# Performance work log

Hardware: AMD Instinct MI355X
Metric: run time of the kernel (lower is better)

## Reference

```python
import jax, jax.numpy as jnp
import numpy as np

IN_SHAPE = 640
LEVELS = [3, 4, 5]          # pyramid_levels [3,5] expanded
REG_LEN = 64
NUM_CLASSES = 80
MAX_OUT = 100
SCORE_TH = 0.3
IOU_TH = 0.5
NEG_INF = -1e30


def _make_anchors():
    """Anchor-free anchors: one box per grid cell, grid_zero_start=True,
    anchor_scale=1, aspect_ratio=1 -> half-size = stride/2. Normalized by input size."""
    all_a = []
    for lvl in LEVELS:
        stride = 2 ** lvl
        fs = IN_SHAPE // stride
        hh = np.arange(fs, dtype='float32') * stride
        ww = np.arange(fs, dtype='float32') * stride
        wg, hg = np.meshgrid(ww, hh)
        centers = np.stack([hg, wg], -1).reshape(-1, 2)  # [fs*fs, 2] (h, w)
        half = stride * 0.5
        all_a.append(np.concatenate([centers - half, centers + half], -1))
    return np.concatenate(all_a, 0) / IN_SHAPE  # [8400, 4]


def setup_inputs() -> dict:
    key = jax.random.key(0)
    preds = jax.random.normal(key, (64, 8400, REG_LEN + NUM_CLASSES), dtype=jnp.float32)
    anchors = jnp.asarray(_make_anchors(), dtype=jnp.float32)
    return {"preds": preds, "anchors": anchors}


def _decode_yolov8(preds, anchors):
    bbox_logits, cls_logits = preds[..., :REG_LEN], preds[..., REG_LEN:]
    B, N = bbox_logits.shape[:2]
    bins = REG_LEN // 4  # 16
    d = bbox_logits.reshape(B, N, 4, bins)
    # softmax-weighted DFL expectation over bins
    d = jnp.sum(jax.nn.softmax(d, axis=-1) * jnp.arange(bins, dtype=d.dtype), axis=-1)  # [B,N,4]
    tl, br = d[..., :2], d[..., 2:]
    anchors_hw = anchors[:, 2:] - anchors[:, :2]          # [N,2]
    anchors_ctr = (anchors[:, :2] + anchors[:, 2:]) * 0.5  # [N,2]
    bc = (br - tl) * 0.5 * anchors_hw + anchors_ctr        # center
    bhw = (br + tl) * anchors_hw                           # height/width
    boxes = jnp.concatenate([bc - bhw * 0.5, bc + bhw * 0.5], -1)  # [B,N,4] corners
    return boxes, cls_logits


def _iou_one_vs_all(box, boxes):
    tl = jnp.maximum(box[:2], boxes[:, :2])
    br = jnp.minimum(box[2:], boxes[:, 2:])
    inter = jnp.prod(jnp.clip(br - tl, 0.0, None), -1)
    a1 = jnp.prod(box[2:] - box[:2])
    a2 = jnp.prod(boxes[:, 2:] - boxes[:, :2], -1)
    return inter / (a1 + a2 - inter + 1e-9)


def _nms_single(boxes, scores):
    """Greedy hard NMS for one image. boxes [N,4], scores [N] -> idxs [MAX_OUT] (-1 = invalid)."""
    n = scores.shape[0]
    sc0 = jnp.where(scores > SCORE_TH, scores, NEG_INF)

    def step(sc, _):
        j = jnp.argmax(sc)
        valid = sc[j] > NEG_INF * 0.5
        idx = jnp.where(valid, j, -1).astype(jnp.int32)
        iou = _iou_one_vs_all(boxes[j], boxes)
        sc = jnp.where((iou > IOU_TH) | (jnp.arange(n) == j), NEG_INF, sc)
        return sc, idx

    _, idxs = jax.lax.scan(step, sc0, None, length=MAX_OUT)
    return idxs


def reference(preds, anchors):
    boxes, cls = _decode_yolov8(preds, anchors)       # [B,N,4], [B,N,C]
    scores = jnp.max(cls, -1)                          # [B,N]
    labels = jnp.argmax(cls, -1).astype(jnp.int32)     # [B,N]
    idxs = jax.vmap(_nms_single)(boxes, scores)        # [B,MAX_OUT]
    valid = idxs >= 0
    safe = jnp.maximum(idxs, 0)
    out_boxes = jnp.take_along_axis(boxes, safe[:, :, None], axis=1) * valid[..., None]
    out_scores = jnp.take_along_axis(scores, safe, axis=1) * valid
    out_labels = jnp.where(valid, jnp.take_along_axis(labels, safe, axis=1), -1)
    return out_boxes, out_labels, out_scores
```

## Files before the change

kernel.cpp:

```cpp
#include <hip/hip_runtime.h>

namespace {
constexpr int kB = 64;
constexpr int kN = 8400;
constexpr int kNP = 16384;
constexpr int kReg = 64;
constexpr int kCls = 80;
constexpr int kStride = kReg + kCls;
constexpr int kMaxOut = 100;
constexpr float kScoreTh = 0.3f;
constexpr float kIouTh = 0.5f;
}

__global__ __launch_bounds__(256) void decode2_k(
    const float* __restrict__ preds,
    const float* __restrict__ anchors,
    float4* __restrict__ boxes,
    float* __restrict__ scores,
    int* __restrict__ labels,
    unsigned long long* __restrict__ keys)
{
    __shared__ float lds[64 * 148];
    const int tid = threadIdx.x;
    const size_t gbase = (size_t)blockIdx.x * 64;

    const float4* src = (const float4*)(preds + gbase * kStride);
    float4* l4 = (float4*)lds;
#pragma unroll
    for (int k = 0; k < 9; ++k) {
        int i = tid + k * 256;
        int row = i / 36, col = i - row * 36;
        l4[row * 37 + col] = src[i];
    }
    __syncthreads();

    const int a = tid >> 2, s = tid & 3;
    const float* rowp = lds + a * 148;

    float x[16];
    const float4* q = (const float4*)(rowp + s * 16);
#pragma unroll
    for (int j = 0; j < 4; ++j) ((float4*)x)[j] = q[j];
    float m = x[0];
#pragma unroll
    for (int j = 1; j < 16; ++j) m = fmaxf(m, x[j]);
    float se = 0.f, we = 0.f;
#pragma unroll
    for (int j = 0; j < 16; ++j) {
        float t = expf(x[j] - m);
        se += t;
        we += t * (float)j;
    }
    float d = we / se;

    const float4* cl = (const float4*)(rowp + kReg + s * 20);
    float bv = -3e38f; int bi = 0;
#pragma unroll
    for (int c = 0; c < 5; ++c) {
        float4 v = cl[c];
        int cb = s * 20 + 4 * c;
        if (v.x > bv) { bv = v.x; bi = cb; }
        if (v.y > bv) { bv = v.y; bi = cb + 1; }
        if (v.z > bv) { bv = v.z; bi = cb + 2; }
        if (v.w > bv) { bv = v.w; bi = cb + 3; }
    }

    const int lane = tid & 63;
    const int base = lane & ~3;
    float d0 = __shfl(d, base + 0, 64);
    float d1 = __shfl(d, base + 1, 64);
    float d2 = __shfl(d, base + 2, 64);
    float d3 = __shfl(d, base + 3, 64);
    float v1 = __shfl(bv, base + 1, 64); int i1 = __shfl(bi, base + 1, 64);
    float v2 = __shfl(bv, base + 2, 64); int i2 = __shfl(bi, base + 2, 64);
    float v3 = __shfl(bv, base + 3, 64); int i3 = __shfl(bi, base + 3, 64);

    if (s == 0) {
        float best = bv; int bl = bi;
        if (v1 > best) { best = v1; bl = i1; }
        if (v2 > best) { best = v2; bl = i2; }
        if (v3 > best) { best = v3; bl = i3; }

        size_t gi = gbase + a;
        int bimg = (int)(gi / kN);
        int n = (int)(gi - (size_t)bimg * kN);
        float4 av = ((const float4*)anchors)[n];
        float ah0 = av.z - av.x, ah1 = av.w - av.y;
        float c0 = (av.x + av.z) * 0.5f, c1 = (av.y + av.w) * 0.5f;
        float bc0 = (d2 - d0) * 0.5f * ah0 + c0;
        float bc1 = (d3 - d1) * 0.5f * ah1 + c1;
        float bh0 = (d2 + d0) * ah0;
        float bh1 = (d3 + d1) * ah1;
        boxes[gi] = make_float4(bc0 - bh0 * 0.5f, bc1 - bh1 * 0.5f,
                                bc0 + bh0 * 0.5f, bc1 + bh1 * 0.5f);
        scores[gi] = best;
        labels[gi] = bl;

        unsigned long long kkey = ~0ULL;
        if (best > kScoreTh) {
            unsigned u = __float_as_uint(best);
            unsigned o = u ^ ((u & 0x80000000u) ? 0xFFFFFFFFu : 0x80000000u);
            kkey = ((unsigned long long)(~o) << 32) | (unsigned)n;
        }
        keys[((size_t)bimg << 14) + n] = kkey;
    }
}

__global__ __launch_bounds__(512) void sortB_k(unsigned long long* __restrict__ keys)
{
    __shared__ unsigned long long lk[8192];
    const int h = blockIdx.x & 1;
    unsigned long long* base = keys + ((size_t)blockIdx.x << 13);
    for (int t = threadIdx.x; t < 8192; t += 512)
        lk[t] = (h * 8192 + t < kN) ? base[t] : ~0ULL;
    __syncthreads();
    for (int size = 2; size <= 8192; size <<= 1) {
        const bool isTop = (size == 8192);
        for (int stride = size >> 1; stride > 0; stride >>= 1) {
#pragma unroll
            for (int p = 0; p < 8; ++p) {
                int n = threadIdx.x + (p << 9);
                int i = ((n & ~(stride - 1)) << 1) | (n & (stride - 1));
                int j = i + stride;
                bool desc = isTop ? (h == 1) : ((i & size) != 0);
                unsigned long long a = lk[i], c = lk[j];
                bool sw = desc ? (c > a) : (a > c);
                if (sw) { lk[i] = c; lk[j] = a; }
            }
            __syncthreads();
        }
    }
    for (int t = threadIdx.x; t < 8192; t += 512) base[t] = lk[t];
}

__global__ __launch_bounds__(256) void sortC_k(unsigned long long* __restrict__ keys)
{
    int t = blockIdx.x * 256 + threadIdx.x;
    int b = t >> 13, i = t & 8191;
    unsigned long long* p = keys + ((size_t)b << 14);
    unsigned long long a = p[i], c = p[i + 8192];
    if (a > c) { p[i] = c; p[i + 8192] = a; }
}

__global__ __launch_bounds__(512) void sortD_k(unsigned long long* __restrict__ keys)
{
    __shared__ unsigned long long lk[8192];
    unsigned long long* base = keys + ((size_t)blockIdx.x << 13);
    for (int t = threadIdx.x; t < 8192; t += 512) lk[t] = base[t];
    __syncthreads();
    for (int stride = 4096; stride > 0; stride >>= 1) {
#pragma unroll
        for (int p = 0; p < 8; ++p) {
            int n = threadIdx.x + (p << 9);
            int i = ((n & ~(stride - 1)) << 1) | (n & (stride - 1));
            int j = i + stride;
            unsigned long long a = lk[i], c = lk[j];
            if (a > c) { lk[i] = c; lk[j] = a; }
        }
        __syncthreads();
    }
    for (int t = threadIdx.x; t < 8192; t += 512) base[t] = lk[t];
}

__global__ __launch_bounds__(256) void nms_k(
    const float4* __restrict__ boxes,
    const float* __restrict__ scores,
    const int* __restrict__ labels,
    const unsigned long long* __restrict__ keys,
    float* __restrict__ out)
{
    __shared__ float4 kbox[kMaxOut];
    __shared__ float karea[kMaxOut];
    __shared__ unsigned long long ball[4];
    __shared__ int firstt, kcS, doneS, stopS;

    const int b = blockIdx.x, tid = threadIdx.x;
    const unsigned long long* sk = keys + ((size_t)b << 14);
    const float4* bx = boxes + (size_t)b * kN;

    if (tid == 0) { kcS = 0; doneS = 0; }

    for (int c = 0; c < kNP / 256; ++c) {
        __syncthreads();
        if (tid == 0) stopS = (sk[c * 256] == ~0ULL);
        unsigned long long key = sk[c * 256 + tid];
        bool alive = (key != ~0ULL);
        int idx = alive ? (int)(key & 0xFFFFFFFFULL) : 0;
        float4 cb = bx[idx];
        float ac = (cb.z - cb.x) * (cb.w - cb.y);
        __syncthreads();
        if (stopS) break;
        int kcl = kcS;
        if (alive) {
            for (int k = 0; k < kcl; ++k) {
                float4 kb = kbox[k];
                float t0 = fmaxf(kb.x, cb.x), t1 = fmaxf(kb.y, cb.y);
                float b0 = fminf(kb.z, cb.z), b1 = fminf(kb.w, cb.w);
                float inter = fmaxf(b0 - t0, 0.f) * fmaxf(b1 - t1, 0.f);
                float iou = inter / (karea[k] + ac - inter + 1e-9f);
                if (iou > kIouTh) { alive = false; break; }
            }
        }
        while (true) {
            unsigned long long mm = __ballot((int)alive);
            if ((tid & 63) == 0) ball[tid >> 6] = mm;
            __syncthreads();
            if (tid == 0) {
                int ft = -1;
                for (int w = 0; w < 4; ++w)
                    if (ball[w]) { ft = (w << 6) + __ffsll(ball[w]) - 1; break; }
                firstt = ft;
            }
            __syncthreads();
            int ft = firstt;
            if (ft < 0) break;
            if (tid == ft) {
                int k = kcS;
                kbox[k] = cb; karea[k] = ac;
                ((float4*)out)[b * kMaxOut + k] = cb;
                out[kB * kMaxOut * 4 + b * kMaxOut + k] =
                    (float)labels[(size_t)b * kN + idx];
                out[kB * kMaxOut * 5 + b * kMaxOut + k] =
                    scores[(size_t)b * kN + idx];
                kcS = k + 1;
                alive = false;
                if (k + 1 == kMaxOut) doneS = 1;
            }
            __syncthreads();
            if (doneS) break;
            int kn = kcS;
            if (alive) {
                float4 kb = kbox[kn - 1];
                float t0 = fmaxf(kb.x, cb.x), t1 = fmaxf(kb.y, cb.y);
                float b0 = fminf(kb.z, cb.z), b1 = fminf(kb.w, cb.w);
                float inter = fmaxf(b0 - t0, 0.f) * fmaxf(b1 - t1, 0.f);
                float iou = inter / (karea[kn - 1] + ac - inter + 1e-9f);
                if (iou > kIouTh) alive = false;
            }
            __syncthreads();
        }
        if (doneS) break;
    }
    __syncthreads();
    int kcf = kcS;
    for (int k = kcf + tid; k < kMaxOut; k += 256) {
        ((float4*)out)[b * kMaxOut + k] = make_float4(0.f, 0.f, 0.f, 0.f);
        out[kB * kMaxOut * 4 + b * kMaxOut + k] = -1.0f;
        out[kB * kMaxOut * 5 + b * kMaxOut + k] = 0.0f;
    }
}

extern "C" void kernel_launch(void* const* d_in, const int* in_sizes, int n_in,
                              void* d_out, int out_size, void* d_ws, size_t ws_size,
                              hipStream_t stream)
{
    const float* preds = (const float*)d_in[0];
    const float* anchors = (const float*)d_in[1];
    float* out = (float*)d_out;

    char* ws = (char*)d_ws;
    float4* boxes = (float4*)ws;
    float* scores = (float*)(ws + (size_t)kB * kN * 16);
    int* labels = (int*)(ws + (size_t)kB * kN * 20);
    unsigned long long* keys =
        (unsigned long long*)(ws + (size_t)kB * kN * 24);

    decode2_k<<<(kB * kN) / 64, 256, 0, stream>>>(preds, anchors, boxes, scores, labels, keys);
    sortB_k<<<kB * 2, 512, 0, stream>>>(keys);
    sortC_k<<<(kB * 8192) / 256, 256, 0, stream>>>(keys);
    sortD_k<<<kB * 2, 512, 0, stream>>>(keys);
    nms_k<<<kB, 256, 0, stream>>>(boxes, scores, labels, keys, out);
}
```

Measured before the change: 603.8 us.

## Replace full 16K bitonic sort with 8K sort plus in-NMS merge of sorted tail

The sort now covers only the first 8192 keys per image in a single kernel, dropping the second half-block sort and the two merge kernels. The NMS kernel sorts the 208-key tail in LDS and merge-path-merges it with the main run 256 keys at a time. It also resolves each chunk's candidates with a single wavefront using ballots instead of block-wide syncs per kept box. This cuts launches and global sort traffic, at the cost of more serial merge and selection logic inside the NMS kernel.

```diff
diff --git a/kernel.cpp b/kernel.cpp
--- a/kernel.cpp
+++ b/kernel.cpp
@@ -3,7 +3,8 @@
 namespace {
 constexpr int kB = 64;
 constexpr int kN = 8400;
-constexpr int kNP = 16384;
+constexpr int kMain = 8192;
+constexpr int kTail = kN - kMain;
 constexpr int kReg = 64;
 constexpr int kCls = 80;
 constexpr int kStride = kReg + kCls;
@@ -109,20 +110,17 @@
 __global__ __launch_bounds__(512) void sortB_k(unsigned long long* __restrict__ keys)
 {
     __shared__ unsigned long long lk[8192];
-    const int h = blockIdx.x & 1;
-    unsigned long long* base = keys + ((size_t)blockIdx.x << 13);
-    for (int t = threadIdx.x; t < 8192; t += 512)
-        lk[t] = (h * 8192 + t < kN) ? base[t] : ~0ULL;
+    unsigned long long* base = keys + ((size_t)blockIdx.x << 14);
+    for (int t = threadIdx.x; t < 8192; t += 512) lk[t] = base[t];
     __syncthreads();
     for (int size = 2; size <= 8192; size <<= 1) {
-        const bool isTop = (size == 8192);
         for (int stride = size >> 1; stride > 0; stride >>= 1) {
 #pragma unroll
             for (int p = 0; p < 8; ++p) {
                 int n = threadIdx.x + (p << 9);
                 int i = ((n & ~(stride - 1)) << 1) | (n & (stride - 1));
                 int j = i + stride;
-                bool desc = isTop ? (h == 1) : ((i & size) != 0);
+                bool desc = (i & size) != 0;
                 unsigned long long a = lk[i], c = lk[j];
                 bool sw = desc ? (c > a) : (a > c);
                 if (sw) { lk[i] = c; lk[j] = a; }
@@ -133,33 +131,11 @@
     for (int t = threadIdx.x; t < 8192; t += 512) base[t] = lk[t];
 }
 
-__global__ __launch_bounds__(256) void sortC_k(unsigned long long* __restrict__ keys)
-{
-    int t = blockIdx.x * 256 + threadIdx.x;
-    int b = t >> 13, i = t & 8191;
-    unsigned long long* p = keys + ((size_t)b << 14);
-    unsigned long long a = p[i], c = p[i + 8192];
-    if (a > c) { p[i] = c; p[i + 8192] = a; }
-}
-
-__global__ __launch_bounds__(512) void sortD_k(unsigned long long* __restrict__ keys)
-{
-    __shared__ unsigned long long lk[8192];
-    unsigned long long* base = keys + ((size_t)blockIdx.x << 13);
-    for (int t = threadIdx.x; t < 8192; t += 512) lk[t] = base[t];
-    __syncthreads();
-    for (int stride = 4096; stride > 0; stride >>= 1) {
-#pragma unroll
-        for (int p = 0; p < 8; ++p) {
-            int n = threadIdx.x + (p << 9);
-            int i = ((n & ~(stride - 1)) << 1) | (n & (stride - 1));
-            int j = i + stride;
-            unsigned long long a = lk[i], c = lk[j];
-            if (a > c) { lk[i] = c; lk[j] = a; }
-        }
-        __syncthreads();
-    }
-    for (int t = threadIdx.x; t < 8192; t += 512) base[t] = lk[t];
+__device__ __forceinline__ unsigned long long getB_(
+    const unsigned long long* tailL, int p1, int x)
+{
+    int t = p1 + x;
+    return (t < 256) ? tailL[t] : ~0ULL;
 }
 
 __global__ __launch_bounds__(256) void nms_k(
@@ -169,84 +145,148 @@
     const unsigned long long* __restrict__ keys,
     float* __restrict__ out)
 {
-    __shared__ float4 kbox[kMaxOut];
-    __shared__ float karea[kMaxOut];
-    __shared__ unsigned long long ball[4];
-    __shared__ int firstt, kcS, doneS, stopS;
+    __shared__ unsigned long long tailL[256];
+    __shared__ unsigned long long aw[512];
+    __shared__ float4 sbox[256];
+    __shared__ float  sar[256];
+    __shared__ int    sidx[256];
+    __shared__ float4 kboxL[kMaxOut];
+    __shared__ float  kareaL[kMaxOut];
+    __shared__ int    kidxL[kMaxOut];
+    __shared__ unsigned long long ballS[4];
+    __shared__ int p0S, p1S, kcS, doneS, stopS;
 
     const int b = blockIdx.x, tid = threadIdx.x;
-    const unsigned long long* sk = keys + ((size_t)b << 14);
+    const unsigned long long* mainA = keys + ((size_t)b << 14);
     const float4* bx = boxes + (size_t)b * kN;
 
-    if (tid == 0) { kcS = 0; doneS = 0; }
-
-    for (int c = 0; c < kNP / 256; ++c) {
+    if (tid == 0) { p0S = 0; p1S = 0; kcS = 0; doneS = 0; }
+
+    tailL[tid] = (tid < kTail) ? mainA[kMain + tid] : ~0ULL;
+    __syncthreads();
+    for (int size = 2; size <= 256; size <<= 1) {
+        for (int stride = size >> 1; stride > 0; stride >>= 1) {
+            if (tid < 128) {
+                int i = ((tid & ~(stride - 1)) << 1) | (tid & (stride - 1));
+                int j = i + stride;
+                bool desc = (i & size) != 0;
+                unsigned long long a = tailL[i], c = tailL[j];
+                bool sw = desc ? (c > a) : (a > c);
+                if (sw) { tailL[i] = c; tailL[j] = a; }
+            }
+            __syncthreads();
+        }
+    }
+
+    int kc = 0;
+    for (int c = 0; c < 33; ++c) {
+        int p0 = p0S, p1 = p1S;
+        aw[tid]       = (p0 + tid       < kMain) ? mainA[p0 + tid]       : ~0ULL;
+        aw[tid + 256] = (p0 + tid + 256 < kMain) ? mainA[p0 + tid + 256] : ~0ULL;
         __syncthreads();
-        if (tid == 0) stopS = (sk[c * 256] == ~0ULL);
-        unsigned long long key = sk[c * 256 + tid];
+
+        int d = tid;
+        int lo = 0, hi = d;
+        while (lo < hi) {
+            int mid = (lo + hi) >> 1;
+            bool c2 = getB_(tailL, p1, d - mid - 1) < aw[mid];
+            if (c2) hi = mid; else lo = mid + 1;
+        }
+        unsigned long long av = aw[lo];
+        unsigned long long bv = getB_(tailL, p1, d - lo);
+        unsigned long long key = (av <= bv) ? av : bv;
+
         bool alive = (key != ~0ULL);
         int idx = alive ? (int)(key & 0xFFFFFFFFULL) : 0;
         float4 cb = bx[idx];
         float ac = (cb.z - cb.x) * (cb.w - cb.y);
-        __syncthreads();
-        if (stopS) break;
-        int kcl = kcS;
+
         if (alive) {
-            for (int k = 0; k < kcl; ++k) {
-                float4 kb = kbox[k];
+            for (int k = 0; k < kc; ++k) {
+                float4 kb = kboxL[k];
                 float t0 = fmaxf(kb.x, cb.x), t1 = fmaxf(kb.y, cb.y);
                 float b0 = fminf(kb.z, cb.z), b1 = fminf(kb.w, cb.w);
                 float inter = fmaxf(b0 - t0, 0.f) * fmaxf(b1 - t1, 0.f);
-                float iou = inter / (karea[k] + ac - inter + 1e-9f);
+                float iou = inter / (kareaL[k] + ac - inter + 1e-9f);
                 if (iou > kIouTh) { alive = false; break; }
             }
         }
-        while (true) {
-            unsigned long long mm = __ballot((int)alive);
-            if ((tid & 63) == 0) ball[tid >> 6] = mm;
-            __syncthreads();
-            if (tid == 0) {
-                int ft = -1;
-                for (int w = 0; w < 4; ++w)
-                    if (ball[w]) { ft = (w << 6) + __ffsll(ball[w]) - 1; break; }
-                firstt = ft;
-            }
-            __syncthreads();
-            int ft = firstt;
-            if (ft < 0) break;
-            if (tid == ft) {
-                int k = kcS;
-                kbox[k] = cb; karea[k] = ac;
-                ((float4*)out)[b * kMaxOut + k] = cb;
-                out[kB * kMaxOut * 4 + b * kMaxOut + k] =
-                    (float)labels[(size_t)b * kN + idx];
-                out[kB * kMaxOut * 5 + b * kMaxOut + k] =
-                    scores[(size_t)b * kN + idx];
-                kcS = k + 1;
-                alive = false;
-                if (k + 1 == kMaxOut) doneS = 1;
-            }
-            __syncthreads();
-            if (doneS) break;
-            int kn = kcS;
-            if (alive) {
-                float4 kb = kbox[kn - 1];
-                float t0 = fmaxf(kb.x, cb.x), t1 = fmaxf(kb.y, cb.y);
-                float b0 = fminf(kb.z, cb.z), b1 = fminf(kb.w, cb.w);
-                float inter = fmaxf(b0 - t0, 0.f) * fmaxf(b1 - t1, 0.f);
-                float iou = inter / (karea[kn - 1] + ac - inter + 1e-9f);
-                if (iou > kIouTh) alive = false;
-            }
-            __syncthreads();
-        }
+        sbox[tid] = cb; sar[tid] = ac; sidx[tid] = idx;
+        unsigned long long mm = __ballot((int)alive);
+        if ((tid & 63) == 0) ballS[tid >> 6] = mm;
+        if (tid == 0) {
+            stopS = (key == ~0ULL);
+            int lo2 = 0, hi2 = 256;
+            while (lo2 < hi2) {
+                int mid = (lo2 + hi2) >> 1;
+                bool c2 = getB_(tailL, p1, 255 - mid) < aw[mid];
+                if (c2) hi2 = mid; else lo2 = mid + 1;
+            }
+            p0S = p0 + lo2; p1S = p1 + (256 - lo2);
+        }
+        __syncthreads();
+        if (stopS) break;
+
+        if (tid < 64) {
+            const int lane = tid;
+            unsigned a4 = 0;
+#pragma unroll
+            for (int j = 0; j < 4; ++j)
+                a4 |= (unsigned)((ballS[j] >> lane) & 1ULL) << j;
+            int kcl = kc;
+            while (true) {
+                int jF = -1, lF = 0;
+#pragma unroll
+                for (int j = 0; j < 4; ++j) {
+                    if (jF < 0) {
+                        unsigned long long m2 = __ballot((int)((a4 >> j) & 1u));
+                        if (m2) { jF = j; lF = __ffsll((unsigned long long)m2) - 1; }
+                    }
+                }
+                if (jF < 0) break;
+                int cs = (jF << 6) + lF;
+                float4 kb = sbox[cs];
+                float kar = sar[cs];
+                if (lane == 0) {
+                    kboxL[kcl] = kb; kareaL[kcl] = kar; kidxL[kcl] = sidx[cs];
+                }
+                if (lane == lF) a4 &= ~(1u << jF);
+                ++kcl;
+                if (kcl == kMaxOut) break;
+#pragma unroll
+                for (int j = 0; j < 4; ++j) {
+                    if ((a4 >> j) & 1u) {
+                        float4 cb2 = sbox[lane + (j << 6)];
+                        float ac2 = sar[lane + (j << 6)];
+                        float t0 = fmaxf(kb.x, cb2.x), t1 = fmaxf(kb.y, cb2.y);
+                        float b0 = fminf(kb.z, cb2.z), b1 = fminf(kb.w, cb2.w);
+                        float inter = fmaxf(b0 - t0, 0.f) * fmaxf(b1 - t1, 0.f);
+                        float iou = inter / (kar + ac2 - inter + 1e-9f);
+                        if (iou > kIouTh) a4 &= ~(1u << j);
+                    }
+                }
+            }
+            if (lane == 0) { kcS = kcl; if (kcl == kMaxOut) doneS = 1; }
+        }
+        __syncthreads();
+        kc = kcS;
         if (doneS) break;
     }
-    __syncthreads();
+
     int kcf = kcS;
-    for (int k = kcf + tid; k < kMaxOut; k += 256) {
-        ((float4*)out)[b * kMaxOut + k] = make_float4(0.f, 0.f, 0.f, 0.f);
-        out[kB * kMaxOut * 4 + b * kMaxOut + k] = -1.0f;
-        out[kB * kMaxOut * 5 + b * kMaxOut + k] = 0.0f;
+    if (tid < kMaxOut) {
+        if (tid < kcf) {
+            int idx = kidxL[tid];
+            ((float4*)out)[b * kMaxOut + tid] = kboxL[tid];
+            out[kB * kMaxOut * 4 + b * kMaxOut + tid] =
+                (float)labels[(size_t)b * kN + idx];
+            out[kB * kMaxOut * 5 + b * kMaxOut + tid] =
+                scores[(size_t)b * kN + idx];
+        } else {
+            ((float4*)out)[b * kMaxOut + tid] = make_float4(0.f, 0.f, 0.f, 0.f);
+            out[kB * kMaxOut * 4 + b * kMaxOut + tid] = -1.0f;
+            out[kB * kMaxOut * 5 + b * kMaxOut + tid] = 0.0f;
+        }
     }
 }
 
@@ -266,8 +306,6 @@
         (unsigned long long*)(ws + (size_t)kB * kN * 24);
 
     decode2_k<<<(kB * kN) / 64, 256, 0, stream>>>(preds, anchors, boxes, scores, labels, keys);
-    sortB_k<<<kB * 2, 512, 0, stream>>>(keys);
-    sortC_k<<<(kB * 8192) / 256, 256, 0, stream>>>(keys);
-    sortD_k<<<kB * 2, 512, 0, stream>>>(keys);
+    sortB_k<<<kB, 512, 0, stream>>>(keys);
     nms_k<<<kB, 256, 0, stream>>>(boxes, scores, labels, keys, out);
 }
```

After: 559.0 us. 1.08x faster.
